# Kernel optimization log

Hardware: AMD Instinct MI355X
Metric: run time of the kernel (lower is better)

Reference implementation:

```python
import jax, jax.numpy as jnp
import numpy as np

B, Q, P, HID, H, KV, D = 2, 1024, 3072, 4096, 32, 8, 128
G = H // KV          # GQA group size
EPS = 1e-6
ROPE_THETA = 1e6


def setup_inputs() -> dict:
    key = jax.random.key(0)
    ks = jax.random.split(key, 8)
    hidden_states = jax.random.normal(ks[0], (B, Q, HID), jnp.float32)
    # real RoPE tables for positions [P, P+Q) (extend phase)
    pos = jnp.arange(P, P + Q, dtype=jnp.float32)
    inv_freq = 1.0 / (ROPE_THETA ** (jnp.arange(0, D, 2, dtype=jnp.float32) / D))
    freqs = pos[:, None] * inv_freq[None, :]            # [Q, D/2]
    emb = jnp.concatenate([freqs, freqs], axis=-1)       # [Q, D]
    cos = jnp.broadcast_to(jnp.cos(emb)[None], (B, Q, D)).astype(jnp.float32)
    sin = jnp.broadcast_to(jnp.sin(emb)[None], (B, Q, D)).astype(jnp.float32)
    k_cache = jax.random.normal(ks[1], (B, KV, P, D), jnp.float32)
    v_cache = jax.random.normal(ks[2], (B, KV, P, D), jnp.float32)
    s = 0.02
    Wq = jax.random.normal(ks[3], (HID, H * D), jnp.float32) * s
    Wk = jax.random.normal(ks[4], (HID, KV * D), jnp.float32) * s
    Wv = jax.random.normal(ks[5], (HID, KV * D), jnp.float32) * s
    Wo = jax.random.normal(ks[6], (H * D, HID), jnp.float32) * s
    q_norm_w = jnp.ones((D,), jnp.float32)
    k_norm_w = jnp.ones((D,), jnp.float32)
    return dict(hidden_states=hidden_states, cos=cos, sin=sin,
                k_cache=k_cache, v_cache=v_cache,
                Wq=Wq, Wk=Wk, Wv=Wv, Wo=Wo,
                q_norm_w=q_norm_w, k_norm_w=k_norm_w)


def _rmsnorm(x, w):
    var = jnp.mean(x * x, axis=-1, keepdims=True)
    return x * jax.lax.rsqrt(var + EPS) * w


def _rotate_half(x):
    x1, x2 = jnp.split(x, 2, axis=-1)
    return jnp.concatenate([-x2, x1], axis=-1)


def _rope(x, cos, sin):
    # x: [B, h, Q, D]; cos/sin: [B, Q, D] -> broadcast over heads
    c = cos[:, None, :, :]
    s = sin[:, None, :, :]
    return x * c + _rotate_half(x) * s


def reference(hidden_states, cos, sin, k_cache, v_cache,
              Wq, Wk, Wv, Wo, q_norm_w, k_norm_w):
    # projections
    q = (hidden_states @ Wq).reshape(B, Q, H, D)
    k = (hidden_states @ Wk).reshape(B, Q, KV, D)
    v = (hidden_states @ Wv).reshape(B, Q, KV, D)
    # per-head RMSNorm on q and k
    q = _rmsnorm(q, q_norm_w)
    k = _rmsnorm(k, k_norm_w)
    # [B, heads, Q, D]
    q = q.transpose(0, 2, 1, 3)
    k = k.transpose(0, 2, 1, 3)
    v = v.transpose(0, 2, 1, 3)
    q = _rope(q, cos, sin)
    k = _rope(k, cos, sin)
    # extend: concat cached prefix KV with new KV -> kv_len = P + Q
    K = jnp.concatenate([k_cache, k], axis=2)   # [B, KV, P+Q, D]
    V = jnp.concatenate([v_cache, v], axis=2)
    qg = q.reshape(B, KV, G, Q, D)
    scale = 1.0 / jnp.sqrt(jnp.float32(D))
    scores = jnp.einsum('bkgqd,bksd->bkgqs', qg, K) * scale  # [B,KV,G,Q,P+Q]
    # causal mask offset by prefix: query i sees keys <= P + i
    key_idx = jnp.arange(P + Q)
    mask = key_idx[None, :] <= (P + jnp.arange(Q))[:, None]  # [Q, P+Q]
    scores = jnp.where(mask[None, None, None], scores, jnp.float32(-1e30))
    attn = jax.nn.softmax(scores, axis=-1)
    out = jnp.einsum('bkgqs,bksd->bkgqd', attn, V)           # [B,KV,G,Q,D]
    out = out.reshape(B, H, Q, D).transpose(0, 2, 1, 3).reshape(B, Q, H * D)
    return out @ Wo
```

## Files before the change

### kernel.cpp

```cpp
#include <hip/hip_runtime.h>
#include <hip/hip_bf16.h>

#define B_ 2
#define Q_ 1024
#define P_ 3072
#define HID_ 4096
#define H_ 32
#define KV_ 8
#define D_ 128
#define S_ 4096
#define NQKV 6144
#define QSCALE 0.1275174432f

typedef __attribute__((ext_vector_type(4))) float f32x4;
typedef __attribute__((ext_vector_type(8))) unsigned short u16x8;
typedef __attribute__((ext_vector_type(4))) unsigned short u16x4;
typedef __attribute__((ext_vector_type(8))) __bf16 bf16x8;

__device__ __forceinline__ unsigned short f2bf(float f){
  unsigned u = __builtin_bit_cast(unsigned, f);
  unsigned r = (u + 0x7FFFu + ((u >> 16) & 1u)) >> 16;
  return (unsigned short)r;
}
__device__ __forceinline__ float bf2f(unsigned short h){
  unsigned u = ((unsigned)h) << 16;
  return __builtin_bit_cast(float, u);
}
__device__ __forceinline__ unsigned pk2bf(float lo, float hi){
  unsigned r;
  asm("v_cvt_pk_bf16_f32 %0, %1, %2" : "=v"(r) : "v"(lo), "v"(hi));
  return r;
}
__device__ __forceinline__ float fexp2(float x){
  float r; asm("v_exp_f32 %0, %1" : "=v"(r) : "v"(x)); return r;
}
__device__ __forceinline__ f32x4 mfma16(u16x8 a, u16x8 b, f32x4 c){
  return __builtin_amdgcn_mfma_f32_16x16x32_bf16(
      __builtin_bit_cast(bf16x8, a), __builtin_bit_cast(bf16x8, b), c, 0, 0, 0);
}
typedef const __attribute__((address_space(1))) void* gp1_t;
typedef __attribute__((address_space(3))) void* lp3_t;
__device__ __forceinline__ void gl16(const unsigned short* g, unsigned short* l){
  __builtin_amdgcn_global_load_lds((gp1_t)g, (lp3_t)l, 16, 0, 0);
}

#define N1_ 2097152
#define N2_ 1572864
__global__ __launch_bounds__(256) void setup(
    const float* __restrict__ hs, const float* __restrict__ kc,
    const float* __restrict__ vc, const float* __restrict__ qw,
    const float* __restrict__ kw, unsigned short* __restrict__ AH,
    unsigned short* __restrict__ Kb, unsigned short* __restrict__ VT,
    float* __restrict__ M){
  __shared__ unsigned short T[128][72];
  __shared__ float sa[4], sb[4];
  int bx = blockIdx.x;
  int tid = threadIdx.x;
  if(bx < 2048){
    const int PD = P_ * D_;
    const long SD = (long)S_ * D_;
    for(int i4 = bx * 256 + tid; i4 < N1_ + N2_; i4 += 2048 * 256){
      if(i4 < N1_){
        long i = (long)i4 * 4;
        float4 x = *(const float4*)(hs + i);
        *(u16x4*)(AH + i) = (u16x4){f2bf(x.x), f2bf(x.y), f2bf(x.z), f2bf(x.w)};
      } else {
        long i = (long)(i4 - N1_) * 4;
        int bkv = (int)(i / PD);
        int rem = (int)(i - (long)bkv * PD);
        long dst = (long)bkv * SD + rem;
        float4 k4 = *(const float4*)(kc + i);
        *(u16x4*)(Kb + dst) = (u16x4){f2bf(k4.x), f2bf(k4.y), f2bf(k4.z), f2bf(k4.w)};
      }
    }
  } else if(bx < 2816){
    int idx = bx - 2048;
    int bkv = idx / 48;
    int s0 = (idx % 48) * 64;
    int r = tid >> 2, dblk = (tid & 3) * 32;
    const float* src = vc + ((long)bkv * P_ + s0 + r) * 128 + dblk;
    #pragma unroll
    for(int u = 0; u < 8; ++u){
      float4 v = *(const float4*)(src + u*4);
      T[dblk + u*4 + 0][r] = f2bf(v.x);
      T[dblk + u*4 + 1][r] = f2bf(v.y);
      T[dblk + u*4 + 2][r] = f2bf(v.z);
      T[dblk + u*4 + 3][r] = f2bf(v.w);
    }
    __syncthreads();
    int d = tid >> 1, sh = (tid & 1) * 32;
    unsigned short* dst = VT + ((long)bkv * 128 + d) * S_ + s0 + sh;
    #pragma unroll
    for(int u = 0; u < 4; ++u){
      u16x8 v;
      #pragma unroll
      for(int j = 0; j < 8; ++j) v[j] = T[d][sh + u*8 + j];
      *(u16x8*)(dst + u*8) = v;
    }
  } else {
    float a = (tid < 128) ? fabsf(qw[tid]) : 0.f;
    float b = (tid < 128) ? fabsf(kw[tid]) : 0.f;
    #pragma unroll
    for(int o = 32; o; o >>= 1){
      a = fmaxf(a, __shfl_xor(a, o));
      b = fmaxf(b, __shfl_xor(b, o));
    }
    if((tid & 63) == 0){ sa[tid >> 6] = a; sb[tid >> 6] = b; }
    __syncthreads();
    if(tid == 0){
      float mq = fmaxf(fmaxf(sa[0], sa[1]), fmaxf(sa[2], sa[3]));
      float mk = fmaxf(fmaxf(sb[0], sb[1]), fmaxf(sb[2], sb[3]));
      M[0] = 128.0f * QSCALE * mq * mk * 1.01f + 0.25f;
    }
  }
}

__global__ __launch_bounds__(256) void convert_w(
    const float* __restrict__ Wq, const float* __restrict__ Wk,
    const float* __restrict__ Wv, const float* __restrict__ Wo,
    unsigned short* __restrict__ WT, unsigned short* __restrict__ WoT){
  __shared__ float tile[64][65];
  int x = blockIdx.x;
  const float* W; int ldn, n_off; unsigned short* dst; int n0;
  if(x < 64)      { W = Wq; ldn = 4096; n_off = 0;    dst = WT;  n0 = x * 64; }
  else if(x < 80) { W = Wk; ldn = 1024; n_off = 4096; dst = WT;  n0 = (x-64) * 64; }
  else if(x < 96) { W = Wv; ldn = 1024; n_off = 5120; dst = WT;  n0 = (x-80) * 64; }
  else            { W = Wo; ldn = 4096; n_off = 0;    dst = WoT; n0 = (x-96) * 64; }
  int k0 = blockIdx.y * 64;
  int tid = threadIdx.x;
  int r = tid >> 4, c = (tid & 15) * 4;
  #pragma unroll
  for(int j = 0; j < 4; ++j){
    float4 v = *(const float4*)(W + (long)(k0 + r + j*16) * ldn + n0 + c);
    tile[r + j*16][c] = v.x; tile[r + j*16][c+1] = v.y;
    tile[r + j*16][c+2] = v.z; tile[r + j*16][c+3] = v.w;
  }
  __syncthreads();
  #pragma unroll
  for(int j = 0; j < 4; ++j){
    int n = r + j*16;
    long o = (long)(n_off + n0 + n) * 4096 + k0 + c;
    *(u16x4*)(dst + o) = (u16x4){f2bf(tile[c][n]), f2bf(tile[c+1][n]),
                                 f2bf(tile[c+2][n]), f2bf(tile[c+3][n])};
  }
}

__global__ __launch_bounds__(256) void gemm_bf16(
    const unsigned short* __restrict__ Ag, const unsigned short* __restrict__ Bg,
    float* __restrict__ C, int nbx, int ldc){
  __shared__ __align__(16) unsigned short sA[4096], sB[4096];
  int tid = threadIdx.x;
  int nwg = nbx * 16;
  int lin = blockIdx.x;
  int cpx = nwg >> 3;
  int swz = (lin & 7) * cpx + (lin >> 3);
  int by = swz & 15, bx = swz >> 4;
  int m0 = by * 128, n0 = bx * 128;
  int lane = tid & 63, w = tid >> 6;
  int lr = lane & 15, lg = lane >> 4;
  int wm = (w >> 1) * 64, wn = (w & 1) * 64;
  int rowi = w * 16 + (lane >> 2);
  int cchunk = ((lane & 3) ^ ((lane >> 3) & 3)) << 3;
  const unsigned short* aP = Ag + (long)(m0 + rowi) * 4096 + cchunk;
  const unsigned short* bP = Bg + (long)(n0 + rowi) * 4096 + cchunk;
  const int step2 = 64 * 4096;
  unsigned short* dA = sA + w * 512;
  unsigned short* dB = sB + w * 512;
  int rdcol = (lg * 8) ^ (((lr >> 1) & 3) << 3);
  f32x4 zero = {0.f,0.f,0.f,0.f};
  f32x4 acc[4][4];
  #pragma unroll
  for(int mi=0;mi<4;++mi)
    #pragma unroll
    for(int ni=0;ni<4;++ni) acc[mi][ni] = zero;

  for(int kt = 0; kt < 128; ++kt){
    int kk = kt * 32;
    __syncthreads();
    gl16(aP + kk, dA);  gl16(aP + step2 + kk, dA + 2048);
    gl16(bP + kk, dB);  gl16(bP + step2 + kk, dB + 2048);
    __syncthreads();
    u16x8 ah[4];
    #pragma unroll
    for(int mi = 0; mi < 4; ++mi)
      ah[mi] = *(const u16x8*)(sA + (wm + mi*16 + lr) * 32 + rdcol);
    #pragma unroll
    for(int ni = 0; ni < 4; ++ni){
      u16x8 bh = *(const u16x8*)(sB + (wn + ni*16 + lr) * 32 + rdcol);
      #pragma unroll
      for(int mi = 0; mi < 4; ++mi)
        acc[mi][ni] = mfma16(ah[mi], bh, acc[mi][ni]);
    }
  }
  #pragma unroll
  for(int mi = 0; mi < 4; ++mi)
    #pragma unroll
    for(int r = 0; r < 4; ++r){
      long rowoff = (long)(m0 + wm + mi*16 + lg*4 + r) * ldc + n0 + wn + lr;
      #pragma unroll
      for(int ni = 0; ni < 4; ++ni)
        C[rowoff + ni*16] = acc[mi][ni][r];
    }
}

__global__ __launch_bounds__(256) void pp_qkv(
    const float* __restrict__ Craw, const float* __restrict__ cosb,
    const float* __restrict__ sinb, const float* __restrict__ qw,
    const float* __restrict__ kw, unsigned short* __restrict__ Qb,
    unsigned short* __restrict__ Kb, unsigned short* __restrict__ VT){
  int rid = blockIdx.x * 4 + (threadIdx.x >> 6);
  int lane = threadIdx.x & 63;
  if(rid < 65536){
    int b = rid >> 15;
    int rem = rid & 32767;
    int q = rem >> 5;
    int h = rem & 31;
    long rowoff = (long)(b * Q_ + q) * NQKV + h * 128;
    float x1 = Craw[rowoff + lane];
    float x2 = Craw[rowoff + 64 + lane];
    float ss = x1*x1 + x2*x2;
    for(int o = 32; o; o >>= 1) ss += __shfl_xor(ss, o);
    float norm = rsqrtf(ss * (1.0f/128.0f) + 1e-6f);
    float xn1 = x1 * norm * qw[lane];
    float xn2 = x2 * norm * qw[64 + lane];
    long co = (long)(b * Q_ + q) * 128;
    float c1 = cosb[co + lane],      s1 = sinb[co + lane];
    float c2 = cosb[co + 64 + lane], s2 = sinb[co + 64 + lane];
    float o1 = (xn1 * c1 - xn2 * s1) * QSCALE;
    float o2 = (xn2 * c2 + xn1 * s2) * QSCALE;
    long dst = ((long)(b * H_ + h) * Q_ + q) * 128;
    Qb[dst + lane] = f2bf(o1);
    Qb[dst + 64 + lane] = f2bf(o2);
  } else {
    int rid2 = rid - 65536;
    int b = rid2 >> 13;
    int rem = rid2 & 8191;
    int q = rem >> 3;
    int kv = rem & 7;
    int bkv = b * KV_ + kv;
    long rowoff = (long)(b * Q_ + q) * NQKV;
    float x1 = Craw[rowoff + 4096 + kv*128 + lane];
    float x2 = Craw[rowoff + 4096 + kv*128 + 64 + lane];
    float ss = x1*x1 + x2*x2;
    for(int o = 32; o; o >>= 1) ss += __shfl_xor(ss, o);
    float norm = rsqrtf(ss * (1.0f/128.0f) + 1e-6f);
    float xn1 = x1 * norm * kw[lane];
    float xn2 = x2 * norm * kw[64 + lane];
    long co = (long)(b * Q_ + q) * 128;
    float c1 = cosb[co + lane],      s1 = sinb[co + lane];
    float c2 = cosb[co + 64 + lane], s2 = sinb[co + 64 + lane];
    long dst = ((long)bkv * S_ + P_ + q) * 128;
    Kb[dst + lane]      = f2bf(xn1 * c1 - xn2 * s1);
    Kb[dst + 64 + lane] = f2bf(xn2 * c2 + xn1 * s2);
    float v1 = Craw[rowoff + 5120 + kv*128 + lane];
    float v2 = Craw[rowoff + 5120 + kv*128 + 64 + lane];
    VT[((long)bkv * 128 + lane) * S_ + P_ + q]      = f2bf(v1);
    VT[((long)bkv * 128 + 64 + lane) * S_ + P_ + q] = f2bf(v2);
  }
}

#define KVB 32
#define PSL 40
__global__ __launch_bounds__(256, 2) void attn(
    const unsigned short* __restrict__ Qg, const unsigned short* __restrict__ Kg,
    const unsigned short* __restrict__ VTg, const float* __restrict__ Mp,
    unsigned short* __restrict__ po, float* __restrict__ pl){
  __shared__ __align__(16) unsigned short Ks[2][KVB*128];
  __shared__ __align__(16) unsigned short Vs[2][128*KVB];
  __shared__ __align__(16) unsigned short Ps[4][64*PSL];
  int tid = threadIdx.x;
  int qb = blockIdx.x >> 1, sp = blockIdx.x & 1;
  int b = blockIdx.z, h = blockIdx.y, q0 = qb * 256;
  int kvh = h >> 2;
  int w = tid >> 6, lane = tid & 63, lr = lane & 15, lg = lane >> 4;
  int q0w = q0 + w * 64;
  float Mv = Mp[0];
  u16x8 qh[4][4];
  #pragma unroll
  for(int mi = 0; mi < 4; ++mi){
    long qbase = ((long)(b * H_ + h) * Q_ + q0w + mi*16 + lr) * 128;
    #pragma unroll
    for(int c = 0; c < 4; ++c)
      qh[mi][c] = *(const u16x8*)(Qg + qbase + c*32 + lg*8);
  }
  f32x4 minit = {-Mv, -Mv, -Mv, -Mv};
  f32x4 o[4][8];
  #pragma unroll
  for(int mi = 0; mi < 4; ++mi)
    #pragma unroll
    for(int i = 0; i < 8; ++i) o[mi][i] = (f32x4){0.f,0.f,0.f,0.f};
  float l[4] = {0.f, 0.f, 0.f, 0.f};
  long kb  = (long)(b * KV_ + kvh) * S_ * 128;
  long vb0 = (long)(b * KV_ + kvh) * 128 * (long)S_;
  int T = 104 + 8 * qb;
  int half = T >> 1;
  int t0 = sp ? half : 0;
  int t1 = sp ? T : half;
  int koff[2], voff[2], ldst[2];
  #pragma unroll
  for(int i = 0; i < 2; ++i){
    int L = (w*2 + i)*64 + lane;
    ldst[i] = L * 8;
    int r = L >> 4, c8 = (L & 15) ^ (r & 7);
    koff[i] = r*128 + c8*8;
    int d = ((L >> 3) << 1) | (L & 1);
    int sm = (L >> 1) & 3;
    int g = (d & 3) ^ ((d >> 2) & 3);
    voff[i] = d * S_ + ((sm ^ g) << 3);
  }
  {
    const unsigned short* kg = Kg + kb + (long)t0 * (KVB*128);
    const unsigned short* vg = VTg + vb0 + t0 * KVB;
    #pragma unroll
    for(int i = 0; i < 2; ++i){
      gl16(kg + koff[i], &Ks[t0 & 1][ldst[i]]);
      gl16(vg + voff[i], &Vs[t0 & 1][ldst[i]]);
    }
  }
  __syncthreads();

  int lr7 = lr & 7;
  int gread = (lr & 3) ^ ((lr >> 2) & 3);
  for(int t = t0; t < t1; ++t){
    int cur = t & 1;
    if(t + 1 < t1){
      int s1 = (t + 1) * KVB;
      const unsigned short* kg = Kg + kb + (long)s1 * 128;
      const unsigned short* vg = VTg + vb0 + s1;
      #pragma unroll
      for(int i = 0; i < 2; ++i){
        gl16(kg + koff[i], &Ks[cur^1][ldst[i]]);
        gl16(vg + voff[i], &Vs[cur^1][ldst[i]]);
      }
    }
    int s0 = t * KVB;
    if(s0 <= P_ + q0w + 63){
      f32x4 pacc[4][2];
      #pragma unroll
      for(int mi = 0; mi < 4; ++mi){ pacc[mi][0] = minit; pacc[mi][1] = minit; }
      __builtin_amdgcn_s_setprio(1);
      #pragma unroll
      for(int c = 0; c < 4; ++c)
        #pragma unroll
        for(int ni = 0; ni < 2; ++ni){
          u16x8 kh = *(const u16x8*)(&Ks[cur][(ni*16 + lr)*128 + (((c*4 + lg) ^ lr7) << 3)]);
          #pragma unroll
          for(int mi = 0; mi < 4; ++mi)
            pacc[mi][ni] = mfma16(kh, qh[mi][c], pacc[mi][ni]);
        }
      __builtin_amdgcn_s_setprio(0);
      if(s0 + KVB - 1 > P_ + q0w){
        #pragma unroll
        for(int mi = 0; mi < 4; ++mi){
          int qrow = q0w + mi*16 + lr;
          #pragma unroll
          for(int ni = 0; ni < 2; ++ni)
            #pragma unroll
            for(int r = 0; r < 4; ++r){
              int skey = s0 + ni*16 + lg*4 + r;
              if(skey > P_ + qrow) pacc[mi][ni][r] = -1e30f;
            }
        }
      }
      #pragma unroll
      for(int mi = 0; mi < 4; ++mi){
        float rs = 0.f;
        #pragma unroll
        for(int ni = 0; ni < 2; ++ni){
          float p0 = fexp2(pacc[mi][ni][0]);
          float p1 = fexp2(pacc[mi][ni][1]);
          float p2 = fexp2(pacc[mi][ni][2]);
          float p3 = fexp2(pacc[mi][ni][3]);
          rs += (p0 + p1) + (p2 + p3);
          uint2 pw; pw.x = pk2bf(p0, p1); pw.y = pk2bf(p2, p3);
          *(uint2*)(&Ps[w][(mi*16 + lr)*PSL + ni*16 + lg*4]) = pw;
        }
        l[mi] += rs;
      }
      u16x8 pa[4];
      #pragma unroll
      for(int mi = 0; mi < 4; ++mi)
        pa[mi] = *(const u16x8*)(&Ps[w][(mi*16 + lr)*PSL + lg*8]);
      __builtin_amdgcn_s_setprio(1);
      #pragma unroll
      for(int ni = 0; ni < 8; ++ni){
        int d = ni*16 + lr;
        int voffr = ((d >> 1) << 6) + ((lg ^ gread) << 4) + ((d & 1) << 3);
        u16x8 vbf = *(const u16x8*)(&Vs[cur][voffr]);
        #pragma unroll
        for(int mi = 0; mi < 4; ++mi)
          o[mi][ni] = mfma16(pa[mi], vbf, o[mi][ni]);
      }
      __builtin_amdgcn_s_setprio(0);
    }
    __syncthreads();
  }
  int bh = b * H_ + h;
  #pragma unroll
  for(int mi = 0; mi < 4; ++mi){
    float lt = l[mi];
    lt += __shfl_xor(lt, 16);
    lt += __shfl_xor(lt, 32);
    #pragma unroll
    for(int r = 0; r < 4; ++r){
      int qrow = q0w + mi*16 + lg*4 + r;
      long obase = ((long)(sp*64 + bh) * Q_ + qrow) * 128;
      #pragma unroll
      for(int ni = 0; ni < 8; ++ni)
        po[obase + ni*16 + lr] = f2bf(o[mi][ni][r]);
    }
    if(lane < 16)
      pl[(sp*64 + bh) * Q_ + q0w + mi*16 + lane] = lt;
  }
}

__global__ __launch_bounds__(256) void combine(
    const unsigned short* __restrict__ po, const float* __restrict__ pl,
    unsigned short* __restrict__ OH){
  int idx = blockIdx.x * 256 + threadIdx.x;
  int row = idx >> 5;
  int d4 = (idx & 31) * 4;
  int bh = row >> 10, q = row & 1023;
  int b = bh >> 5, h = bh & 31;
  float lsum = pl[bh*1024 + q] + pl[65536 + bh*1024 + q];
  float inv = 1.0f / lsum;
  u16x4 a = *(const u16x4*)(po + (long)row*128 + d4);
  u16x4 c = *(const u16x4*)(po + 8388608L + (long)row*128 + d4);
  u16x4 r = { f2bf((bf2f(a[0]) + bf2f(c[0])) * inv), f2bf((bf2f(a[1]) + bf2f(c[1])) * inv),
              f2bf((bf2f(a[2]) + bf2f(c[2])) * inv), f2bf((bf2f(a[3]) + bf2f(c[3])) * inv) };
  *(u16x4*)(OH + ((long)(b*1024 + q))*4096 + h*128 + d4) = r;
}

extern "C" void kernel_launch(void* const* d_in, const int* in_sizes, int n_in,
                              void* d_out, int out_size, void* d_ws, size_t ws_size,
                              hipStream_t stream){
  const float* hs   = (const float*)d_in[0];
  const float* cosb = (const float*)d_in[1];
  const float* sinb = (const float*)d_in[2];
  const float* kc   = (const float*)d_in[3];
  const float* vc   = (const float*)d_in[4];
  const float* Wq   = (const float*)d_in[5];
  const float* Wk   = (const float*)d_in[6];
  const float* Wv   = (const float*)d_in[7];
  const float* Wo   = (const float*)d_in[8];
  const float* qw   = (const float*)d_in[9];
  const float* kw   = (const float*)d_in[10];
  char* ws = (char*)d_ws;
  float* Craw          = (float*)ws;
  unsigned short* OH   = (unsigned short*)ws;
  unsigned short* WT   = (unsigned short*)(ws + 50331648);
  unsigned short* PO   = (unsigned short*)(ws + 50331648);
  unsigned short* WoT  = (unsigned short*)(ws + 117440512);
  unsigned short* AH   = (unsigned short*)(ws + 150994944);
  unsigned short* QB   = (unsigned short*)(ws + 150994944);
  unsigned short* KB   = (unsigned short*)(ws + 167772160);
  unsigned short* VT   = (unsigned short*)(ws + 184549376);
  float* PL            = (float*)(ws + 201326592);
  float* MW            = (float*)(ws + 201981952);
  float* Out = (float*)d_out;

  setup<<<dim3(2817), dim3(256), 0, stream>>>(hs, kc, vc, qw, kw, AH, KB, VT, MW);
  convert_w<<<dim3(160, 64), dim3(256), 0, stream>>>(Wq, Wk, Wv, Wo, WT, WoT);
  gemm_bf16<<<dim3(768), dim3(256), 0, stream>>>(AH, WT, Craw, 48, NQKV);
  pp_qkv<<<dim3(20480), dim3(256), 0, stream>>>(Craw, cosb, sinb, qw, kw, QB, KB, VT);
  attn<<<dim3(8, 32, 2), dim3(256), 0, stream>>>(QB, KB, VT, MW, PO, PL);
  combine<<<dim3(8192), dim3(256), 0, stream>>>(PO, PL, OH);
  gemm_bf16<<<dim3(512), dim3(256), 0, stream>>>(OH, WoT, Out, 32, 4096);
}
```

Baseline: 485.5 us.

## Add 256x256-tile 8-wave QKV GEMM with 4-stage LDS pipeline

Replaces the 128x128-tile QKV projection GEMM with a dedicated kernel using 256x256 output tiles, 512 threads and a four-deep ring of LDS buffers filled by direct global-to-LDS loads. Loads are interleaved between two MFMA phases, with barriers and setprio to overlap memory with matrix math. The aim is more data reuse per tile and better latency hiding. In exchange it launches only 192 workgroups, which may underfill the 256 CUs, and it needs a large LDS footprint and many accumulator registers.

```diff
diff --git a/kernel.cpp b/kernel.cpp
--- a/kernel.cpp
+++ b/kernel.cpp
@@ -143,6 +143,102 @@
     *(u16x4*)(dst + o) = (u16x4){f2bf(tile[c][n]), f2bf(tile[c+1][n]),
                                  f2bf(tile[c+2][n]), f2bf(tile[c+3][n])};
   }
+}
+
+__global__ __launch_bounds__(512) void gemm_qkv8(
+    const unsigned short* __restrict__ Ag, const unsigned short* __restrict__ Bg,
+    float* __restrict__ C){
+  __shared__ __align__(16) unsigned short LA[4][8192];
+  __shared__ __align__(16) unsigned short LB[4][8192];
+  int tid = threadIdx.x;
+  int lin = blockIdx.x;
+  int swz = (lin & 7) * 24 + (lin >> 3);
+  int by = swz & 7, bx = swz >> 3;
+  int m0 = by * 256, n0 = bx * 256;
+  int lane = tid & 63, w = tid >> 6;
+  int lr = lane & 15, lg = lane >> 4;
+  int wm = (w >> 2) * 128, wn = (w & 3) * 64;
+  const unsigned short* sa0; const unsigned short* sa1;
+  const unsigned short* sb0; const unsigned short* sb1;
+  int sl0, sl1;
+  {
+    int s = tid;
+    int row = s >> 2, kc = (s & 3) ^ ((row >> 1) & 3);
+    sa0 = Ag + (long)(m0 + row) * 4096 + kc * 8;
+    sb0 = Bg + (long)(n0 + row) * 4096 + kc * 8;
+    sl0 = s * 8;
+    s = tid + 512;
+    row = s >> 2; kc = (s & 3) ^ ((row >> 1) & 3);
+    sa1 = Ag + (long)(m0 + row) * 4096 + kc * 8;
+    sb1 = Bg + (long)(n0 + row) * 4096 + kc * 8;
+    sl1 = s * 8;
+  }
+  f32x4 acc[8][4];
+  #pragma unroll
+  for(int mf = 0; mf < 8; ++mf)
+    #pragma unroll
+    for(int nf = 0; nf < 4; ++nf) acc[mf][nf] = (f32x4){0.f,0.f,0.f,0.f};
+  int rdc8 = (lg ^ ((lr >> 1) & 3)) * 8;
+  #pragma unroll
+  for(int tt = 0; tt < 3; ++tt){
+    gl16(sa0 + tt*32, &LA[tt][sl0]);
+    gl16(sa1 + tt*32, &LA[tt][sl1]);
+    gl16(sb0 + tt*32, &LB[tt][sl0]);
+    gl16(sb1 + tt*32, &LB[tt][sl1]);
+  }
+  for(int t = 0; t < 128; ++t){
+    int cb = t & 3;
+    int tt = (t + 3 < 128) ? (t + 3) : 127;
+    int sbuf = (t + 3) & 3;
+    asm volatile("s_waitcnt vmcnt(8)" ::: "memory");
+    __builtin_amdgcn_s_barrier();
+    u16x8 af[4], bf[4];
+    #pragma unroll
+    for(int mf = 0; mf < 4; ++mf)
+      af[mf] = *(const u16x8*)(&LA[cb][(wm + mf*16 + lr)*32 + rdc8]);
+    #pragma unroll
+    for(int nf = 0; nf < 4; ++nf)
+      bf[nf] = *(const u16x8*)(&LB[cb][(wn + nf*16 + lr)*32 + rdc8]);
+    gl16(sa0 + tt*32, &LA[sbuf][sl0]);
+    gl16(sa1 + tt*32, &LA[sbuf][sl1]);
+    __builtin_amdgcn_s_barrier();
+    asm volatile("s_waitcnt lgkmcnt(0)" ::: "memory");
+    __builtin_amdgcn_sched_barrier(0);
+    __builtin_amdgcn_s_setprio(1);
+    #pragma unroll
+    for(int nf = 0; nf < 4; ++nf)
+      #pragma unroll
+      for(int mf = 0; mf < 4; ++mf)
+        acc[mf][nf] = mfma16(af[mf], bf[nf], acc[mf][nf]);
+    __builtin_amdgcn_s_setprio(0);
+    __builtin_amdgcn_s_barrier();
+    u16x8 ag[4];
+    #pragma unroll
+    for(int mf = 0; mf < 4; ++mf)
+      ag[mf] = *(const u16x8*)(&LA[cb][(wm + (mf+4)*16 + lr)*32 + rdc8]);
+    gl16(sb0 + tt*32, &LB[sbuf][sl0]);
+    gl16(sb1 + tt*32, &LB[sbuf][sl1]);
+    __builtin_amdgcn_s_barrier();
+    asm volatile("s_waitcnt lgkmcnt(0)" ::: "memory");
+    __builtin_amdgcn_sched_barrier(0);
+    __builtin_amdgcn_s_setprio(1);
+    #pragma unroll
+    for(int nf = 0; nf < 4; ++nf)
+      #pragma unroll
+      for(int mf = 0; mf < 4; ++mf)
+        acc[4+mf][nf] = mfma16(ag[mf], bf[nf], acc[4+mf][nf]);
+    __builtin_amdgcn_s_setprio(0);
+    __builtin_amdgcn_s_barrier();
+  }
+  #pragma unroll
+  for(int mf = 0; mf < 8; ++mf)
+    #pragma unroll
+    for(int r = 0; r < 4; ++r){
+      long rowoff = (long)(m0 + wm + mf*16 + lg*4 + r) * NQKV + n0 + wn + lr;
+      #pragma unroll
+      for(int nf = 0; nf < 4; ++nf)
+        C[rowoff + nf*16] = acc[mf][nf][r];
+    }
 }
 
 __global__ __launch_bounds__(256) void gemm_bf16(
@@ -461,7 +557,7 @@
 
   setup<<<dim3(2817), dim3(256), 0, stream>>>(hs, kc, vc, qw, kw, AH, KB, VT, MW);
   convert_w<<<dim3(160, 64), dim3(256), 0, stream>>>(Wq, Wk, Wv, Wo, WT, WoT);
-  gemm_bf16<<<dim3(768), dim3(256), 0, stream>>>(AH, WT, Craw, 48, NQKV);
+  gemm_qkv8<<<dim3(192), dim3(512), 0, stream>>>(AH, WT, Craw);
   pp_qkv<<<dim3(20480), dim3(256), 0, stream>>>(Craw, cosb, sinb, qw, kw, QB, KB, VT);
   attn<<<dim3(8, 32, 2), dim3(256), 0, stream>>>(QB, KB, VT, MW, PO, PL);
   combine<<<dim3(8192), dim3(256), 0, stream>>>(PO, PL, OH);
```

Measured after the change: 496.3 us. 2.2% more time.
